# Kernel tuning notes

Hardware: AMD Instinct MI355X
Metric: run time of the kernel (lower is better)

## Reference

```python
import jax, jax.numpy as jnp
import numpy as np

N, NFEAT, NHID, NCLASS, HEADS, NLAYERS, E = 10000, 128, 64, 16, 4, 4, 160000
DT = 0.01
EPS = 1e-05


def _rmsnorm(x):
    rms = jnp.sqrt(jnp.mean(x * x, axis=-1, keepdims=True) + EPS)
    return x / rms


def setup_inputs() -> dict:
    key = jax.random.key(0)
    ks = jax.random.split(key, 16)
    s = lambda fi, fo: 1.0 / np.sqrt(fi)
    def lin(k, fi, fo):
        k1, k2 = jax.random.split(k)
        lim = 1.0 / np.sqrt(fi)
        return (jax.random.uniform(k1, (fi, fo), jnp.float32, -lim, lim),
                jax.random.uniform(k2, (fo,), jnp.float32, -lim, lim))
    x = jax.random.normal(ks[0], (N, NFEAT), jnp.float32)
    edge_index = jax.random.randint(ks[1], (2, E), 0, N, dtype=jnp.int64)
    enc_w, enc_b = lin(ks[2], NFEAT, NHID)
    dec_w, dec_b = lin(ks[3], NHID, NCLASS)
    lo_w, lo_b = lin(ks[4], NHID * HEADS, NHID)
    dpl_w, dpl_b = lin(ks[5], NHID, NHID * HEADS)
    dpr_w, dpr_b = lin(ks[6], NHID, NHID * HEADS)
    lin_w, lin_b = lin(ks[7], NHID, NHID * HEADS)
    att = jax.random.normal(ks[8], (HEADS, NHID), jnp.float32) * (1.0 / np.sqrt(NHID))
    return dict(x=x, enc_w=enc_w, enc_b=enc_b, dec_w=dec_w, dec_b=dec_b,
                lo_w=lo_w, lo_b=lo_b, dpl_w=dpl_w, dpl_b=dpl_b,
                dpr_w=dpr_w, dpr_b=dpr_b, lin_w=lin_w, lin_b=lin_b,
                att=att, edge_index=edge_index)


def reference(x, enc_w, enc_b, dec_w, dec_b, lo_w, lo_b, dpl_w, dpl_b,
              dpr_w, dpr_b, lin_w, lin_b, att, edge_index):
    row, col = edge_index[0], edge_index[1]  # src, dst

    # dynamics constants (learnable_dyn_params=False)
    omega = jax.nn.softplus(jnp.float32(1.0))
    zeta = jax.nn.softplus(jnp.float32(1.0))
    Ks = jax.nn.softplus(jnp.float32(1.0))
    omega_sq = omega * omega

    Y = jax.nn.relu(x @ enc_w + enc_b)              # [N, nhid]
    X = Y

    # fixed GATv2 attention projections from Y_0
    xl = (Y @ dpl_w + dpl_b).reshape(N, HEADS, NHID)  # [N,H,C]
    xr = (Y @ dpr_w + dpr_b).reshape(N, HEADS, NHID)

    # symmetric GCN normalization on edges
    deg = jax.ops.segment_sum(jnp.ones((E,), jnp.float32), col, num_segments=N)
    dis = jnp.where(deg > 0, deg ** -0.5, 0.0)
    norm = dis[row] * dis[col]                       # [E]

    # edge attention logits are fixed across layers (depend only on Y_0)
    e_feat = jax.nn.leaky_relu(xl[row] + xr[col], 0.2)      # [E,H,C]
    score = jnp.einsum('ehc,hc->eh', e_feat, att)           # [E,H]
    smax = jax.ops.segment_max(score, col, num_segments=N)  # [N,H]
    a = jnp.exp(score - smax[col])
    ssum = jax.ops.segment_sum(a, col, num_segments=N)      # [N,H]
    alpha = a / jnp.where(ssum[col] > 0, ssum[col], 1.0)    # [E,H]
    w_edge = alpha * norm[:, None]                          # [E,H]

    for _ in range(NLAYERS):
        v = (Y @ lin_w + lin_b).reshape(N, HEADS, NHID)     # value projection
        msg = v[row] * w_edge[:, :, None]                   # [E,H,C]
        coupling = jax.ops.segment_sum(msg, col, num_segments=N).reshape(N, HEADS * NHID)
        coupling_Y = coupling @ lo_w + lo_b                 # [N, nhid]
        Y = Y + DT * (-2.0 * zeta * omega * Y - omega_sq * X + Ks * coupling_Y)
        X = X + DT * Y
        X = _rmsnorm(X)
        Y = _rmsnorm(Y)

    return X @ dec_w + dec_b                                # [N, nclass]
```

## Files before the change

kernel.cpp:

```cpp
#include <hip/hip_runtime.h>
#include <math.h>

#define NFEAT 128
#define HC    256
#define NCLS  16
#define DT_F  0.01f
#define EPS_F 1e-5f

__device__ __forceinline__ float bf2f(unsigned short u) {
  union { unsigned int u; float f; } v; v.u = ((unsigned int)u) << 16; return v.f;
}
__device__ __forceinline__ unsigned short f2bf(float f) {
  union { float f; unsigned int u; } v; v.f = f;
  unsigned int r = v.u + 0x7fffu + ((v.u >> 16) & 1u);
  return (unsigned short)(r >> 16);
}
__device__ __forceinline__ float edge_logit(ushort4 u, float4 r4, float4 at4) {
  float vx = bf2f(u.x) + r4.x, vy = bf2f(u.y) + r4.y;
  float vz = bf2f(u.z) + r4.z, vw = bf2f(u.w) + r4.w;
  vx = fmaxf(vx, 0.2f * vx); vy = fmaxf(vy, 0.2f * vy);
  vz = fmaxf(vz, 0.2f * vz); vw = fmaxf(vw, 0.2f * vw);
  float t = vx * at4.x;
  t = fmaf(vy, at4.y, t); t = fmaf(vz, at4.z, t); t = fmaf(vw, at4.w, t);
  return t;
}

__global__ __launch_bounds__(256) void enc_kernel(
    const float* __restrict__ x, const float* __restrict__ w,
    const float* __restrict__ b, float* __restrict__ Y, float* __restrict__ X,
    unsigned short* __restrict__ Ybf, int* __restrict__ deg, int n) {
  __shared__ float ws[NFEAT * 64];
  const int gtid = blockIdx.x * 256 + threadIdx.x, GSZ = gridDim.x * 256;
  for (int t = gtid; t < n; t += GSZ) deg[t] = 0;
  for (int t = threadIdx.x; t < NFEAT * 64; t += blockDim.x) ws[t] = w[t];
  __syncthreads();
  const int wave = threadIdx.x >> 6, lane = threadIdx.x & 63;
  for (int i = blockIdx.x * 4 + wave; i < n; i += gridDim.x * 4) {
    const float* xr = x + (size_t)i * NFEAT;
    float acc = b[lane];
#pragma unroll 8
    for (int k = 0; k < NFEAT; ++k) acc = fmaf(xr[k], ws[k * 64 + lane], acc);
    acc = fmaxf(acc, 0.f);
    const size_t idx = (size_t)i * 64 + lane;
    Y[idx] = acc; X[idx] = acc; Ybf[idx] = f2bf(acc);
  }
}

__global__ __launch_bounds__(256) void proj_kernel(
    const float* __restrict__ Y,
    const float* __restrict__ wl, const float* __restrict__ bl,
    const float* __restrict__ wr, const float* __restrict__ br,
    unsigned short* __restrict__ xlb, float* __restrict__ xr, int n) {
  const int half = gridDim.x >> 1;
  const bool doR = (int)blockIdx.x < half;
  const int bid = doR ? blockIdx.x : blockIdx.x - half;
  const float* __restrict__ W = doR ? wr : wl;
  const float* __restrict__ B = doR ? br : bl;
  float wreg[64];
  const int t = threadIdx.x;
#pragma unroll
  for (int k = 0; k < 64; ++k) wreg[k] = W[k * HC + t];
  const float bias = B[t];
  for (int i0 = bid * 4; i0 < n; i0 += half * 4) {
    const float* ap = Y + (size_t)i0 * 64;
    float a0 = bias, a1 = bias, a2 = bias, a3 = bias;
#pragma unroll
    for (int k = 0; k < 64; ++k) {
      const float w = wreg[k];
      a0 = fmaf(ap[k], w, a0);
      a1 = fmaf(ap[64 + k], w, a1);
      a2 = fmaf(ap[128 + k], w, a2);
      a3 = fmaf(ap[192 + k], w, a3);
    }
    if (doR) {
      if (i0 + 0 < n) xr[(size_t)(i0 + 0) * HC + t] = a0;
      if (i0 + 1 < n) xr[(size_t)(i0 + 1) * HC + t] = a1;
      if (i0 + 2 < n) xr[(size_t)(i0 + 2) * HC + t] = a2;
      if (i0 + 3 < n) xr[(size_t)(i0 + 3) * HC + t] = a3;
    } else {
      if (i0 + 0 < n) xlb[(size_t)(i0 + 0) * HC + t] = f2bf(a0);
      if (i0 + 1 < n) xlb[(size_t)(i0 + 1) * HC + t] = f2bf(a1);
      if (i0 + 2 < n) xlb[(size_t)(i0 + 2) * HC + t] = f2bf(a2);
      if (i0 + 3 < n) xlb[(size_t)(i0 + 3) * HC + t] = f2bf(a3);
    }
  }
}

__global__ __launch_bounds__(256) void wextdeg_kernel(
    const int* __restrict__ col, const float* __restrict__ lin_w,
    const float* __restrict__ lin_b, const float* __restrict__ lo_w,
    float* __restrict__ Wext, float* __restrict__ bb, int* __restrict__ deg, int E) {
  const int gtid = blockIdx.x * 256 + threadIdx.x;
  const int GSZ = gridDim.x * 256;
  for (int e = gtid; e < E; e += GSZ) atomicAdd(&deg[col[e]], 1);
  for (int f = gtid; f < 260 * 64; f += GSZ) {
    const int b = f >> 6, j = f & 63;
    float a = 0.f;
    if (b < 256) {
      const int k = b >> 2, h = b & 3;
#pragma unroll 8
      for (int c = 0; c < 64; ++c)
        a = fmaf(lin_w[k * HC + h * 64 + c], lo_w[(size_t)(h * 64 + c) * 64 + j], a);
      Wext[b * 64 + j] = a;
    } else {
      const int h = b - 256;
#pragma unroll 8
      for (int c = 0; c < 64; ++c)
        a = fmaf(lin_b[h * 64 + c], lo_w[(size_t)(h * 64 + c) * 64 + j], a);
      bb[h * 64 + j] = a;
    }
  }
}

__global__ __launch_bounds__(1024) void scan_kernel(
    const int* __restrict__ deg, int* __restrict__ offsets, int* __restrict__ cursor,
    float* __restrict__ dis, int n) {
  __shared__ int part[1024];
  const int t = threadIdx.x;
  const int chunk = (n + 1023) / 1024;
  const int start = t * chunk;
  const int end = min(start + chunk, n);
  int s = 0;
  for (int i = start; i < end; ++i) s += deg[i];
  part[t] = s;
  __syncthreads();
  for (int off = 1; off < 1024; off <<= 1) {
    int v = (t >= off) ? part[t - off] : 0;
    __syncthreads();
    part[t] += v;
    __syncthreads();
  }
  int run = (t == 0) ? 0 : part[t - 1];
  for (int i = start; i < end; ++i) {
    offsets[i] = run;
    cursor[i] = run;
    const int d = deg[i];
    dis[i] = (d > 0) ? rsqrtf((float)d) : 0.f;
    run += d;
  }
}

__global__ __launch_bounds__(256) void scatter_kernel(
    const int* __restrict__ row, const int* __restrict__ col,
    int* __restrict__ cursor, int* __restrict__ srow, int E) {
  int e = blockIdx.x * blockDim.x + threadIdx.x;
  if (e >= E) return;
  int pos = atomicAdd(&cursor[col[e]], 1);
  srow[pos] = row[e];
}

__global__ __launch_bounds__(256) void score_layer1(
    const int* __restrict__ offs, const int* __restrict__ deg,
    const int* __restrict__ srow,
    const unsigned short* __restrict__ xlb, const float* __restrict__ xr,
    const float* __restrict__ att, const float* __restrict__ dis,
    const float* __restrict__ bb, const float* __restrict__ lo_b,
    const float* __restrict__ Wext, const unsigned short* __restrict__ ybf_in,
    const float* __restrict__ Yin, float* __restrict__ Yout,
    unsigned short* __restrict__ ybf_out, float* __restrict__ X,
    float4* __restrict__ sw, float4* __restrict__ invq, float* __restrict__ fb,
    int n, float c_decay, float c_x, float c_k) {
  const int tid = threadIdx.x, wave = tid >> 6, lane = tid & 63;
  float wreg[64];
#pragma unroll
  for (int q = 0; q < 64; ++q) wreg[q] = Wext[(wave * 64 + q) * 64 + lane];
  __shared__ float aggl[4][HC];
  __shared__ float partl[4][4][64];
  const float4 at4 = ((const float4*)att)[lane];
  const ushort4* xlb4 = (const ushort4*)xlb;
  const float4* xr4 = (const float4*)xr;
  const int i = blockIdx.x * 4 + wave;
  float g0 = 0.f, g1 = 0.f, g2 = 0.f, g3 = 0.f;
  float fbv = 0.f;
  if (i < n) {
    const int s = offs[i], e = s + deg[i];
    if (s >= e) {
      if (lane == 0) invq[i] = make_float4(0.f, 0.f, 0.f, 0.f);
      fbv = lo_b[lane];
      fb[(size_t)i * 64 + lane] = fbv;
    } else {
      const float4 r4 = xr4[(size_t)i * 64 + lane];
      const float dd = dis[i];
      float ssum = 0.f, wsum = 0.f;
      int p = s;
      int n0 = 0, n1 = 0, n2 = 0, n3 = 0;
      if (p + 3 < e) { n0 = srow[p]; n1 = srow[p + 1]; n2 = srow[p + 2]; n3 = srow[p + 3]; }
      while (p + 3 < e) {
        const int q0 = n0, q1 = n1, q2 = n2, q3 = n3;
        const int pn = p + 4;
        if (pn + 3 < e) { n0 = srow[pn]; n1 = srow[pn + 1]; n2 = srow[pn + 2]; n3 = srow[pn + 3]; }
        const ushort4 u0 = xlb4[(size_t)q0 * 64 + lane];
        const ushort4 u1 = xlb4[(size_t)q1 * 64 + lane];
        const ushort4 u2 = xlb4[(size_t)q2 * 64 + lane];
        const ushort4 u3 = xlb4[(size_t)q3 * 64 + lane];
        const float di0 = dis[q0], di1 = dis[q1], di2 = dis[q2], di3 = dis[q3];
        const float ya = bf2f(ybf_in[(size_t)q0 * 64 + lane]);
        const float yb = bf2f(ybf_in[(size_t)q1 * 64 + lane]);
        const float yc = bf2f(ybf_in[(size_t)q2 * 64 + lane]);
        const float yd = bf2f(ybf_in[(size_t)q3 * 64 + lane]);
        float t0 = edge_logit(u0, r4, at4);
        float t1 = edge_logit(u1, r4, at4);
        float t2 = edge_logit(u2, r4, at4);
        float t3 = edge_logit(u3, r4, at4);
#pragma unroll
        for (int m = 1; m < 16; m <<= 1) {
          t0 += __shfl_xor(t0, m);
          t1 += __shfl_xor(t1, m);
          t2 += __shfl_xor(t2, m);
          t3 += __shfl_xor(t3, m);
        }
        const float a0 = __expf(t0), a1 = __expf(t1), a2 = __expf(t2), a3 = __expf(t3);
        ssum += (a0 + a1) + (a2 + a3);
        const float sv0 = a0 * di0, sv1 = a1 * di1, sv2 = a2 * di2, sv3 = a3 * di3;
        wsum += (sv0 + sv1) + (sv2 + sv3);
        if ((lane & 15) == 0) {
          ((float*)&sw[p])[lane >> 4] = sv0;
          ((float*)&sw[p + 1])[lane >> 4] = sv1;
          ((float*)&sw[p + 2])[lane >> 4] = sv2;
          ((float*)&sw[p + 3])[lane >> 4] = sv3;
        }
        const float sa0 = __shfl(sv0, 0), sa1 = __shfl(sv0, 16);
        const float sa2 = __shfl(sv0, 32), sa3 = __shfl(sv0, 48);
        g0 = fmaf(sa0, ya, g0); g1 = fmaf(sa1, ya, g1);
        g2 = fmaf(sa2, ya, g2); g3 = fmaf(sa3, ya, g3);
        const float sb0 = __shfl(sv1, 0), sb1 = __shfl(sv1, 16);
        const float sb2 = __shfl(sv1, 32), sb3 = __shfl(sv1, 48);
        g0 = fmaf(sb0, yb, g0); g1 = fmaf(sb1, yb, g1);
        g2 = fmaf(sb2, yb, g2); g3 = fmaf(sb3, yb, g3);
        const float sc0 = __shfl(sv2, 0), sc1 = __shfl(sv2, 16);
        const float sc2 = __shfl(sv2, 32), sc3 = __shfl(sv2, 48);
        g0 = fmaf(sc0, yc, g0); g1 = fmaf(sc1, yc, g1);
        g2 = fmaf(sc2, yc, g2); g3 = fmaf(sc3, yc, g3);
        const float sd0 = __shfl(sv3, 0), sd1 = __shfl(sv3, 16);
        const float sd2 = __shfl(sv3, 32), sd3 = __shfl(sv3, 48);
        g0 = fmaf(sd0, yd, g0); g1 = fmaf(sd1, yd, g1);
        g2 = fmaf(sd2, yd, g2); g3 = fmaf(sd3, yd, g3);
        p = pn;
      }
      for (; p < e; ++p) {
        const int ra = srow[p];
        const ushort4 u0 = xlb4[(size_t)ra * 64 + lane];
        const float dia = dis[ra];
        const float ya = bf2f(ybf_in[(size_t)ra * 64 + lane]);
        float t0 = edge_logit(u0, r4, at4);
#pragma unroll
        for (int m = 1; m < 16; m <<= 1) t0 += __shfl_xor(t0, m);
        const float a0 = __expf(t0);
        ssum += a0;
        const float sv0 = a0 * dia;
        wsum += sv0;
        if ((lane & 15) == 0) ((float*)&sw[p])[lane >> 4] = sv0;
        const float sa0 = __shfl(sv0, 0), sa1 = __shfl(sv0, 16);
        const float sa2 = __shfl(sv0, 32), sa3 = __shfl(sv0, 48);
        g0 = fmaf(sa0, ya, g0); g1 = fmaf(sa1, ya, g1);
        g2 = fmaf(sa2, ya, g2); g3 = fmaf(sa3, ya, g3);
      }
      const float inv = dd / (ssum > 0.f ? ssum : 1.f);
      if ((lane & 15) == 0) ((float*)&invq[i])[lane >> 4] = inv;
      const float i0h = __shfl(inv, 0), i1h = __shfl(inv, 16);
      const float i2h = __shfl(inv, 32), i3h = __shfl(inv, 48);
      g0 *= i0h; g1 *= i1h; g2 *= i2h; g3 *= i3h;
      const float wqv = wsum * inv;
      const float w0 = __shfl(wqv, 0), w1 = __shfl(wqv, 16);
      const float w2 = __shfl(wqv, 32), w3 = __shfl(wqv, 48);
      fbv = lo_b[lane];
      fbv = fmaf(w0, bb[lane], fbv);
      fbv = fmaf(w1, bb[64 + lane], fbv);
      fbv = fmaf(w2, bb[128 + lane], fbv);
      fbv = fmaf(w3, bb[192 + lane], fbv);
      fb[(size_t)i * 64 + lane] = fbv;
    }
  }
  float4 o; o.x = g0; o.y = g1; o.z = g2; o.w = g3;
  ((float4*)aggl[wave])[lane] = o;
  __syncthreads();
  float p0 = 0.f, p1 = 0.f, p2 = 0.f, p3 = 0.f;
#pragma unroll
  for (int q4 = 0; q4 < 16; ++q4) {
    const float4 b0 = *(const float4*)(&aggl[0][wave * 64 + q4 * 4]);
    const float4 b1 = *(const float4*)(&aggl[1][wave * 64 + q4 * 4]);
    const float4 b2 = *(const float4*)(&aggl[2][wave * 64 + q4 * 4]);
    const float4 b3 = *(const float4*)(&aggl[3][wave * 64 + q4 * 4]);
    const float w0 = wreg[q4 * 4], w1 = wreg[q4 * 4 + 1];
    const float w2 = wreg[q4 * 4 + 2], w3 = wreg[q4 * 4 + 3];
    p0 = fmaf(b0.x, w0, p0); p0 = fmaf(b0.y, w1, p0);
    p0 = fmaf(b0.z, w2, p0); p0 = fmaf(b0.w, w3, p0);
    p1 = fmaf(b1.x, w0, p1); p1 = fmaf(b1.y, w1, p1);
    p1 = fmaf(b1.z, w2, p1); p1 = fmaf(b1.w, w3, p1);
    p2 = fmaf(b2.x, w0, p2); p2 = fmaf(b2.y, w1, p2);
    p2 = fmaf(b2.z, w2, p2); p2 = fmaf(b2.w, w3, p2);
    p3 = fmaf(b3.x, w0, p3); p3 = fmaf(b3.y, w1, p3);
    p3 = fmaf(b3.z, w2, p3); p3 = fmaf(b3.w, w3, p3);
  }
  partl[wave][0][lane] = p0;
  partl[wave][1][lane] = p1;
  partl[wave][2][lane] = p2;
  partl[wave][3][lane] = p3;
  __syncthreads();
  if (i < n) {
    const size_t idx = (size_t)i * 64 + lane;
    float outv = fbv;
    outv += partl[0][wave][lane] + partl[1][wave][lane] +
            partl[2][wave][lane] + partl[3][wave][lane];
    const float y = Yin[idx], xv = X[idx];
    const float yn = fmaf(c_k, outv, fmaf(c_x, xv, c_decay * y));
    const float xn = fmaf(DT_F, yn, xv);
    float sy = yn * yn, sx = xn * xn;
#pragma unroll
    for (int m = 32; m > 0; m >>= 1) {
      sy += __shfl_xor(sy, m);
      sx += __shfl_xor(sx, m);
    }
    const float ynn = yn * rsqrtf(sy * (1.f / 64.f) + EPS_F);
    Yout[idx] = ynn;
    ybf_out[idx] = f2bf(ynn);
    X[idx] = xn * rsqrtf(sx * (1.f / 64.f) + EPS_F);
  }
}

__global__ __launch_bounds__(256) void layer_fused(
    const int* __restrict__ offs, const int* __restrict__ deg,
    const int* __restrict__ srow,
    const float4* __restrict__ sw, const float4* __restrict__ invq,
    const unsigned short* __restrict__ ybf_in, const float* __restrict__ Wext,
    const float* __restrict__ fb, const float* __restrict__ Yin,
    float* __restrict__ Yout, unsigned short* __restrict__ ybf_out,
    float* __restrict__ X, int n, float c_decay, float c_x, float c_k) {
  const int t = threadIdx.x, tr = t >> 6, lane = t & 63;
  float wreg[64];
#pragma unroll
  for (int q = 0; q < 64; ++q) wreg[q] = Wext[(tr * 64 + q) * 64 + lane];
  __shared__ float aggl[4][HC];
  __shared__ float partl[4][4][64];
  const int i = blockIdx.x * 4 + tr;
  float4 o = make_float4(0.f, 0.f, 0.f, 0.f);
  if (i < n) {
    const int s = offs[i], e = s + deg[i];
    float a0 = 0.f, a1 = 0.f, a2 = 0.f, a3 = 0.f;
    int p = s;
    int n0 = 0, n1 = 0, n2 = 0, n3 = 0;
    if (p + 3 < e) { n0 = srow[p]; n1 = srow[p + 1]; n2 = srow[p + 2]; n3 = srow[p + 3]; }
    while (p + 3 < e) {
      const int q0 = n0, q1 = n1, q2 = n2, q3 = n3;
      const int pn = p + 4;
      if (pn + 3 < e) { n0 = srow[pn]; n1 = srow[pn + 1]; n2 = srow[pn + 2]; n3 = srow[pn + 3]; }
      const float4 v0 = sw[p], v1 = sw[p + 1], v2 = sw[p + 2], v3 = sw[p + 3];
      const float y0 = bf2f(ybf_in[(size_t)q0 * 64 + lane]);
      const float y1 = bf2f(ybf_in[(size_t)q1 * 64 + lane]);
      const float y2 = bf2f(ybf_in[(size_t)q2 * 64 + lane]);
      const float y3 = bf2f(ybf_in[(size_t)q3 * 64 + lane]);
      a0 = fmaf(v0.x, y0, a0); a1 = fmaf(v0.y, y0, a1);
      a2 = fmaf(v0.z, y0, a2); a3 = fmaf(v0.w, y0, a3);
      a0 = fmaf(v1.x, y1, a0); a1 = fmaf(v1.y, y1, a1);
      a2 = fmaf(v1.z, y1, a2); a3 = fmaf(v1.w, y1, a3);
      a0 = fmaf(v2.x, y2, a0); a1 = fmaf(v2.y, y2, a1);
      a2 = fmaf(v2.z, y2, a2); a3 = fmaf(v2.w, y2, a3);
      a0 = fmaf(v3.x, y3, a0); a1 = fmaf(v3.y, y3, a1);
      a2 = fmaf(v3.z, y3, a2); a3 = fmaf(v3.w, y3, a3);
      p = pn;
    }
    for (; p < e; ++p) {
      const int r0 = srow[p];
      const float4 v0 = sw[p];
      const float y0 = bf2f(ybf_in[(size_t)r0 * 64 + lane]);
      a0 = fmaf(v0.x, y0, a0); a1 = fmaf(v0.y, y0, a1);
      a2 = fmaf(v0.z, y0, a2); a3 = fmaf(v0.w, y0, a3);
    }
    const float4 iv = invq[i];
    o.x = a0 * iv.x; o.y = a1 * iv.y; o.z = a2 * iv.z; o.w = a3 * iv.w;
  }
  ((float4*)aggl[tr])[lane] = o;
  __syncthreads();
  float p0 = 0.f, p1 = 0.f, p2 = 0.f, p3 = 0.f;
#pragma unroll
  for (int q4 = 0; q4 < 16; ++q4) {
    const float4 b0 = *(const float4*)(&aggl[0][tr * 64 + q4 * 4]);
    const float4 b1 = *(const float4*)(&aggl[1][tr * 64 + q4 * 4]);
    const float4 b2 = *(const float4*)(&aggl[2][tr * 64 + q4 * 4]);
    const float4 b3 = *(const float4*)(&aggl[3][tr * 64 + q4 * 4]);
    const float w0 = wreg[q4 * 4], w1 = wreg[q4 * 4 + 1];
    const float w2 = wreg[q4 * 4 + 2], w3 = wreg[q4 * 4 + 3];
    p0 = fmaf(b0.x, w0, p0); p0 = fmaf(b0.y, w1, p0);
    p0 = fmaf(b0.z, w2, p0); p0 = fmaf(b0.w, w3, p0);
    p1 = fmaf(b1.x, w0, p1); p1 = fmaf(b1.y, w1, p1);
    p1 = fmaf(b1.z, w2, p1); p1 = fmaf(b1.w, w3, p1);
    p2 = fmaf(b2.x, w0, p2); p2 = fmaf(b2.y, w1, p2);
    p2 = fmaf(b2.z, w2, p2); p2 = fmaf(b2.w, w3, p2);
    p3 = fmaf(b3.x, w0, p3); p3 = fmaf(b3.y, w1, p3);
    p3 = fmaf(b3.z, w2, p3); p3 = fmaf(b3.w, w3, p3);
  }
  partl[tr][0][lane] = p0;
  partl[tr][1][lane] = p1;
  partl[tr][2][lane] = p2;
  partl[tr][3][lane] = p3;
  __syncthreads();
  if (i < n) {
    const size_t idx = (size_t)i * 64 + lane;
    float outv = fb[idx];
    outv += partl[0][tr][lane] + partl[1][tr][lane] +
            partl[2][tr][lane] + partl[3][tr][lane];
    const float y = Yin[idx], xv = X[idx];
    const float yn = fmaf(c_k, outv, fmaf(c_x, xv, c_decay * y));
    const float xn = fmaf(DT_F, yn, xv);
    float sy = yn * yn, sx = xn * xn;
#pragma unroll
    for (int m = 32; m > 0; m >>= 1) {
      sy += __shfl_xor(sy, m);
      sx += __shfl_xor(sx, m);
    }
    const float ynn = yn * rsqrtf(sy * (1.f / 64.f) + EPS_F);
    Yout[idx] = ynn;
    ybf_out[idx] = f2bf(ynn);
    X[idx] = xn * rsqrtf(sx * (1.f / 64.f) + EPS_F);
  }
}

__global__ __launch_bounds__(256) void layer_last_dec(
    const int* __restrict__ offs, const int* __restrict__ deg,
    const int* __restrict__ srow,
    const float4* __restrict__ sw, const float4* __restrict__ invq,
    const unsigned short* __restrict__ ybf_in, const float* __restrict__ Wext,
    const float* __restrict__ fb, const float* __restrict__ Yin,
    const float* __restrict__ X,
    const float* __restrict__ dec_w, const float* __restrict__ dec_b,
    float* __restrict__ out, int n, float c_decay, float c_x, float c_k) {
  const int t = threadIdx.x, tr = t >> 6, lane = t & 63;
  float wreg[64];
#pragma unroll
  for (int q = 0; q < 64; ++q) wreg[q] = Wext[(tr * 64 + q) * 64 + lane];
  __shared__ float aggl[4][HC];
  __shared__ float partl[4][4][64];
  const int i = blockIdx.x * 4 + tr;
  float4 o = make_float4(0.f, 0.f, 0.f, 0.f);
  if (i < n) {
    const int s = offs[i], e = s + deg[i];
    float a0 = 0.f, a1 = 0.f, a2 = 0.f, a3 = 0.f;
    int p = s;
    int n0 = 0, n1 = 0, n2 = 0, n3 = 0;
    if (p + 3 < e) { n0 = srow[p]; n1 = srow[p + 1]; n2 = srow[p + 2]; n3 = srow[p + 3]; }
    while (p + 3 < e) {
      const int q0 = n0, q1 = n1, q2 = n2, q3 = n3;
      const int pn = p + 4;
      if (pn + 3 < e) { n0 = srow[pn]; n1 = srow[pn + 1]; n2 = srow[pn + 2]; n3 = srow[pn + 3]; }
      const float4 v0 = sw[p], v1 = sw[p + 1], v2 = sw[p + 2], v3 = sw[p + 3];
      const float y0 = bf2f(ybf_in[(size_t)q0 * 64 + lane]);
      const float y1 = bf2f(ybf_in[(size_t)q1 * 64 + lane]);
      const float y2 = bf2f(ybf_in[(size_t)q2 * 64 + lane]);
      const float y3 = bf2f(ybf_in[(size_t)q3 * 64 + lane]);
      a0 = fmaf(v0.x, y0, a0); a1 = fmaf(v0.y, y0, a1);
      a2 = fmaf(v0.z, y0, a2); a3 = fmaf(v0.w, y0, a3);
      a0 = fmaf(v1.x, y1, a0); a1 = fmaf(v1.y, y1, a1);
      a2 = fmaf(v1.z, y1, a2); a3 = fmaf(v1.w, y1, a3);
      a0 = fmaf(v2.x, y2, a0); a1 = fmaf(v2.y, y2, a1);
      a2 = fmaf(v2.z, y2, a2); a3 = fmaf(v2.w, y2, a3);
      a0 = fmaf(v3.x, y3, a0); a1 = fmaf(v3.y, y3, a1);
      a2 = fmaf(v3.z, y3, a2); a3 = fmaf(v3.w, y3, a3);
      p = pn;
    }
    for (; p < e; ++p) {
      const int r0 = srow[p];
      const float4 v0 = sw[p];
      const float y0 = bf2f(ybf_in[(size_t)r0 * 64 + lane]);
      a0 = fmaf(v0.x, y0, a0); a1 = fmaf(v0.y, y0, a1);
      a2 = fmaf(v0.z, y0, a2); a3 = fmaf(v0.w, y0, a3);
    }
    const float4 iv = invq[i];
    o.x = a0 * iv.x; o.y = a1 * iv.y; o.z = a2 * iv.z; o.w = a3 * iv.w;
  }
  ((float4*)aggl[tr])[lane] = o;
  __syncthreads();
  float p0 = 0.f, p1 = 0.f, p2 = 0.f, p3 = 0.f;
#pragma unroll
  for (int q4 = 0; q4 < 16; ++q4) {
    const float4 b0 = *(const float4*)(&aggl[0][tr * 64 + q4 * 4]);
    const float4 b1 = *(const float4*)(&aggl[1][tr * 64 + q4 * 4]);
    const float4 b2 = *(const float4*)(&aggl[2][tr * 64 + q4 * 4]);
    const float4 b3 = *(const float4*)(&aggl[3][tr * 64 + q4 * 4]);
    const float w0 = wreg[q4 * 4], w1 = wreg[q4 * 4 + 1];
    const float w2 = wreg[q4 * 4 + 2], w3 = wreg[q4 * 4 + 3];
    p0 = fmaf(b0.x, w0, p0); p0 = fmaf(b0.y, w1, p0);
    p0 = fmaf(b0.z, w2, p0); p0 = fmaf(b0.w, w3, p0);
    p1 = fmaf(b1.x, w0, p1); p1 = fmaf(b1.y, w1, p1);
    p1 = fmaf(b1.z, w2, p1); p1 = fmaf(b1.w, w3, p1);
    p2 = fmaf(b2.x, w0, p2); p2 = fmaf(b2.y, w1, p2);
    p2 = fmaf(b2.z, w2, p2); p2 = fmaf(b2.w, w3, p2);
    p3 = fmaf(b3.x, w0, p3); p3 = fmaf(b3.y, w1, p3);
    p3 = fmaf(b3.z, w2, p3); p3 = fmaf(b3.w, w3, p3);
  }
  partl[tr][0][lane] = p0;
  partl[tr][1][lane] = p1;
  partl[tr][2][lane] = p2;
  partl[tr][3][lane] = p3;
  __syncthreads();
  if (i < n) {
    const size_t idx = (size_t)i * 64 + lane;
    float outv = fb[idx];
    outv += partl[0][tr][lane] + partl[1][tr][lane] +
            partl[2][tr][lane] + partl[3][tr][lane];
    const float y = Yin[idx], xv = X[idx];
    const float yn = fmaf(c_k, outv, fmaf(c_x, xv, c_decay * y));
    const float xn = fmaf(DT_F, yn, xv);
    float sx = xn * xn;
#pragma unroll
    for (int m = 32; m > 0; m >>= 1) sx += __shfl_xor(sx, m);
    const float xnn = xn * rsqrtf(sx * (1.f / 64.f) + EPS_F);
    aggl[tr][lane] = xnn;
    const int j = lane & 15, kq = lane >> 4;
    float a = 0.f;
#pragma unroll
    for (int k2 = 0; k2 < 16; ++k2) {
      const int k = kq * 16 + k2;
      a = fmaf(aggl[tr][k], dec_w[k * NCLS + j], a);
    }
    a += __shfl_xor(a, 16);
    a += __shfl_xor(a, 32);
    if (lane < 16) out[(size_t)i * NCLS + lane] = a + dec_b[lane];
  }
}

static inline size_t alignup(size_t x) { return (x + 255) & ~(size_t)255; }

extern "C" void kernel_launch(void* const* d_in, const int* in_sizes, int n_in,
                              void* d_out, int out_size, void* d_ws, size_t ws_size,
                              hipStream_t stream) {
  const float* x     = (const float*)d_in[0];
  const float* enc_w = (const float*)d_in[1];
  const float* enc_b = (const float*)d_in[2];
  const float* dec_w = (const float*)d_in[3];
  const float* dec_b = (const float*)d_in[4];
  const float* lo_w  = (const float*)d_in[5];
  const float* lo_b  = (const float*)d_in[6];
  const float* dpl_w = (const float*)d_in[7];
  const float* dpl_b = (const float*)d_in[8];
  const float* dpr_w = (const float*)d_in[9];
  const float* dpr_b = (const float*)d_in[10];
  const float* lin_w = (const float*)d_in[11];
  const float* lin_b = (const float*)d_in[12];
  const float* att   = (const float*)d_in[13];
  const int*   ei    = (const int*)d_in[14];

  const int n = in_sizes[0] / NFEAT;
  const int E = in_sizes[14] / 2;
  const int* row = ei;
  const int* col = ei + E;

  char* p = (char*)d_ws;
  size_t off = 0;
  auto alloc = [&](size_t bytes) { void* r = p + off; off += alignup(bytes); return r; };
  float*          Y    = (float*)alloc((size_t)n * 64 * 4);
  float*          Y2   = (float*)alloc((size_t)n * 64 * 4);
  float*          X    = (float*)alloc((size_t)n * 64 * 4);
  unsigned short* ybfA = (unsigned short*)alloc((size_t)n * 64 * 2);
  unsigned short* ybfB = (unsigned short*)alloc((size_t)n * 64 * 2);
  unsigned short* xlb  = (unsigned short*)alloc((size_t)n * HC * 2);
  float*          xr   = (float*)alloc((size_t)n * HC * 4);
  float4*         sw   = (float4*)alloc((size_t)E * 16);
  int*            srow = (int*)alloc((size_t)E * 4);
  int*            deg  = (int*)alloc((size_t)n * 4);
  int*            offs = (int*)alloc((size_t)(n + 1) * 4);
  int*            cur  = (int*)alloc((size_t)n * 4);
  float*          dis  = (float*)alloc((size_t)n * 4);
  float4*         invq = (float4*)alloc((size_t)n * 16);
  float*          fb   = (float*)alloc((size_t)n * 64 * 4);
  float*          Wext = (float*)alloc((size_t)HC * 64 * 4);
  float*          bb   = (float*)alloc((size_t)HC * 4);

  const double sp = log1p(exp(1.0));
  const float c_decay = (float)(1.0 - 2.0 * sp * sp * 0.01);
  const float c_x     = (float)(-(sp * sp) * 0.01);
  const float c_k     = (float)(sp * 0.01);

  const int quads = (n + 3) / 4;

  enc_kernel<<<512, 256, 0, stream>>>(x, enc_w, enc_b, Y, X, ybfA, deg, n);
  proj_kernel<<<1024, 256, 0, stream>>>(Y, dpl_w, dpl_b, dpr_w, dpr_b, xlb, xr, n);
  wextdeg_kernel<<<512, 256, 0, stream>>>(col, lin_w, lin_b, lo_w, Wext, bb, deg, E);
  scan_kernel<<<1, 1024, 0, stream>>>(deg, offs, cur, dis, n);
  scatter_kernel<<<(E + 255) / 256, 256, 0, stream>>>(row, col, cur, srow, E);
  score_layer1<<<quads, 256, 0, stream>>>(offs, deg, srow, xlb, xr, att, dis, bb, lo_b,
                                          Wext, ybfA, Y, Y2, ybfB, X, sw, invq, fb,
                                          n, c_decay, c_x, c_k);
  layer_fused<<<quads, 256, 0, stream>>>(offs, deg, srow, sw, invq, ybfB, Wext, fb,
                                         Y2, Y, ybfA, X, n, c_decay, c_x, c_k);
  layer_fused<<<quads, 256, 0, stream>>>(offs, deg, srow, sw, invq, ybfA, Wext, fb,
                                         Y, Y2, ybfB, X, n, c_decay, c_x, c_k);
  layer_last_dec<<<quads, 256, 0, stream>>>(offs, deg, srow, sw, invq, ybfB, Wext, fb,
                                            Y2, X, dec_w, dec_b, (float*)d_out,
                                            n, c_decay, c_x, c_k);
}
```

Baseline: 202.4 us.

## Store gathered Y and xl features in fp8 and merge weight-prep into projection kernel

Changes the gathered per-node buffers (Y copies and the xl attention projection) from bf16 to fp8 e4m3 using the hardware convert builtins, halving gather bytes in the edge-aggregation kernels. Also folds the degree counting and the Wext/bb weight precompute into the projection kernel, removing one launch. Fp8 cuts precision on the attention logits and messages, which may push outputs past the tolerance.

```diff
diff --git a/kernel.cpp b/kernel.cpp
--- a/kernel.cpp
+++ b/kernel.cpp
@@ -7,17 +7,21 @@
 #define DT_F  0.01f
 #define EPS_F 1e-5f
 
-__device__ __forceinline__ float bf2f(unsigned short u) {
-  union { unsigned int u; float f; } v; v.u = ((unsigned int)u) << 16; return v.f;
-}
-__device__ __forceinline__ unsigned short f2bf(float f) {
-  union { float f; unsigned int u; } v; v.f = f;
-  unsigned int r = v.u + 0x7fffu + ((v.u >> 16) & 1u);
-  return (unsigned short)(r >> 16);
-}
-__device__ __forceinline__ float edge_logit(ushort4 u, float4 r4, float4 at4) {
-  float vx = bf2f(u.x) + r4.x, vy = bf2f(u.y) + r4.y;
-  float vz = bf2f(u.z) + r4.z, vw = bf2f(u.w) + r4.w;
+__device__ __forceinline__ unsigned char f2f8(float f) {
+  int v = __builtin_amdgcn_cvt_pk_fp8_f32(f, f, 0, false);
+  return (unsigned char)(v & 0xff);
+}
+__device__ __forceinline__ float f82f(unsigned int b) {
+  return __builtin_amdgcn_cvt_f32_fp8((int)b, 0);
+}
+__device__ __forceinline__ float f82f_sel0(unsigned int w) { return __builtin_amdgcn_cvt_f32_fp8((int)w, 0); }
+__device__ __forceinline__ float f82f_sel1(unsigned int w) { return __builtin_amdgcn_cvt_f32_fp8((int)w, 1); }
+__device__ __forceinline__ float f82f_sel2(unsigned int w) { return __builtin_amdgcn_cvt_f32_fp8((int)w, 2); }
+__device__ __forceinline__ float f82f_sel3(unsigned int w) { return __builtin_amdgcn_cvt_f32_fp8((int)w, 3); }
+
+__device__ __forceinline__ float edge_logit(unsigned int w, float4 r4, float4 at4) {
+  float vx = f82f_sel0(w) + r4.x, vy = f82f_sel1(w) + r4.y;
+  float vz = f82f_sel2(w) + r4.z, vw = f82f_sel3(w) + r4.w;
   vx = fmaxf(vx, 0.2f * vx); vy = fmaxf(vy, 0.2f * vy);
   vz = fmaxf(vz, 0.2f * vz); vw = fmaxf(vw, 0.2f * vw);
   float t = vx * at4.x;
@@ -28,7 +32,7 @@
 __global__ __launch_bounds__(256) void enc_kernel(
     const float* __restrict__ x, const float* __restrict__ w,
     const float* __restrict__ b, float* __restrict__ Y, float* __restrict__ X,
-    unsigned short* __restrict__ Ybf, int* __restrict__ deg, int n) {
+    unsigned char* __restrict__ Ybf, int* __restrict__ deg, int n) {
   __shared__ float ws[NFEAT * 64];
   const int gtid = blockIdx.x * 256 + threadIdx.x, GSZ = gridDim.x * 256;
   for (int t = gtid; t < n; t += GSZ) deg[t] = 0;
@@ -42,7 +46,7 @@
     for (int k = 0; k < NFEAT; ++k) acc = fmaf(xr[k], ws[k * 64 + lane], acc);
     acc = fmaxf(acc, 0.f);
     const size_t idx = (size_t)i * 64 + lane;
-    Y[idx] = acc; X[idx] = acc; Ybf[idx] = f2bf(acc);
+    Y[idx] = acc; X[idx] = acc; Ybf[idx] = f2f8(acc);
   }
 }
 
@@ -50,7 +54,11 @@
     const float* __restrict__ Y,
     const float* __restrict__ wl, const float* __restrict__ bl,
     const float* __restrict__ wr, const float* __restrict__ br,
-    unsigned short* __restrict__ xlb, float* __restrict__ xr, int n) {
+    const int* __restrict__ col, const float* __restrict__ lin_w,
+    const float* __restrict__ lin_b, const float* __restrict__ lo_w,
+    unsigned char* __restrict__ xlb, float* __restrict__ xr,
+    float* __restrict__ Wext, float* __restrict__ bb, int* __restrict__ deg,
+    int n, int E) {
   const int half = gridDim.x >> 1;
   const bool doR = (int)blockIdx.x < half;
   const int bid = doR ? blockIdx.x : blockIdx.x - half;
@@ -78,32 +86,25 @@
       if (i0 + 2 < n) xr[(size_t)(i0 + 2) * HC + t] = a2;
       if (i0 + 3 < n) xr[(size_t)(i0 + 3) * HC + t] = a3;
     } else {
-      if (i0 + 0 < n) xlb[(size_t)(i0 + 0) * HC + t] = f2bf(a0);
-      if (i0 + 1 < n) xlb[(size_t)(i0 + 1) * HC + t] = f2bf(a1);
-      if (i0 + 2 < n) xlb[(size_t)(i0 + 2) * HC + t] = f2bf(a2);
-      if (i0 + 3 < n) xlb[(size_t)(i0 + 3) * HC + t] = f2bf(a3);
-    }
-  }
-}
-
-__global__ __launch_bounds__(256) void wextdeg_kernel(
-    const int* __restrict__ col, const float* __restrict__ lin_w,
-    const float* __restrict__ lin_b, const float* __restrict__ lo_w,
-    float* __restrict__ Wext, float* __restrict__ bb, int* __restrict__ deg, int E) {
-  const int gtid = blockIdx.x * 256 + threadIdx.x;
-  const int GSZ = gridDim.x * 256;
+      if (i0 + 0 < n) xlb[(size_t)(i0 + 0) * HC + t] = f2f8(a0);
+      if (i0 + 1 < n) xlb[(size_t)(i0 + 1) * HC + t] = f2f8(a1);
+      if (i0 + 2 < n) xlb[(size_t)(i0 + 2) * HC + t] = f2f8(a2);
+      if (i0 + 3 < n) xlb[(size_t)(i0 + 3) * HC + t] = f2f8(a3);
+    }
+  }
+  const int gtid = blockIdx.x * 256 + t, GSZ = gridDim.x * 256;
   for (int e = gtid; e < E; e += GSZ) atomicAdd(&deg[col[e]], 1);
   for (int f = gtid; f < 260 * 64; f += GSZ) {
-    const int b = f >> 6, j = f & 63;
+    const int b2 = f >> 6, j = f & 63;
     float a = 0.f;
-    if (b < 256) {
-      const int k = b >> 2, h = b & 3;
+    if (b2 < 256) {
+      const int k = b2 >> 2, h = b2 & 3;
 #pragma unroll 8
       for (int c = 0; c < 64; ++c)
         a = fmaf(lin_w[k * HC + h * 64 + c], lo_w[(size_t)(h * 64 + c) * 64 + j], a);
-      Wext[b * 64 + j] = a;
+      Wext[b2 * 64 + j] = a;
     } else {
-      const int h = b - 256;
+      const int h = b2 - 256;
 #pragma unroll 8
       for (int c = 0; c < 64; ++c)
         a = fmaf(lin_b[h * 64 + c], lo_w[(size_t)(h * 64 + c) * 64 + j], a);
@@ -152,12 +153,12 @@
 __global__ __launch_bounds__(256) void score_layer1(
     const int* __restrict__ offs, const int* __restrict__ deg,
     const int* __restrict__ srow,
-    const unsigned short* __restrict__ xlb, const float* __restrict__ xr,
+    const unsigned char* __restrict__ xlb, const float* __restrict__ xr,
     const float* __restrict__ att, const float* __restrict__ dis,
     const float* __restrict__ bb, const float* __restrict__ lo_b,
-    const float* __restrict__ Wext, const unsigned short* __restrict__ ybf_in,
+    const float* __restrict__ Wext, const unsigned char* __restrict__ ybf_in,
     const float* __restrict__ Yin, float* __restrict__ Yout,
-    unsigned short* __restrict__ ybf_out, float* __restrict__ X,
+    unsigned char* __restrict__ ybf_out, float* __restrict__ X,
     float4* __restrict__ sw, float4* __restrict__ invq, float* __restrict__ fb,
     int n, float c_decay, float c_x, float c_k) {
   const int tid = threadIdx.x, wave = tid >> 6, lane = tid & 63;
@@ -167,7 +168,7 @@
   __shared__ float aggl[4][HC];
   __shared__ float partl[4][4][64];
   const float4 at4 = ((const float4*)att)[lane];
-  const ushort4* xlb4 = (const ushort4*)xlb;
+  const unsigned int* xlb4 = (const unsigned int*)xlb;
   const float4* xr4 = (const float4*)xr;
   const int i = blockIdx.x * 4 + wave;
   float g0 = 0.f, g1 = 0.f, g2 = 0.f, g3 = 0.f;
@@ -189,15 +190,15 @@
         const int q0 = n0, q1 = n1, q2 = n2, q3 = n3;
         const int pn = p + 4;
         if (pn + 3 < e) { n0 = srow[pn]; n1 = srow[pn + 1]; n2 = srow[pn + 2]; n3 = srow[pn + 3]; }
-        const ushort4 u0 = xlb4[(size_t)q0 * 64 + lane];
-        const ushort4 u1 = xlb4[(size_t)q1 * 64 + lane];
-        const ushort4 u2 = xlb4[(size_t)q2 * 64 + lane];
-        const ushort4 u3 = xlb4[(size_t)q3 * 64 + lane];
+        const unsigned int u0 = xlb4[(size_t)q0 * 64 + lane];
+        const unsigned int u1 = xlb4[(size_t)q1 * 64 + lane];
+        const unsigned int u2 = xlb4[(size_t)q2 * 64 + lane];
+        const unsigned int u3 = xlb4[(size_t)q3 * 64 + lane];
         const float di0 = dis[q0], di1 = dis[q1], di2 = dis[q2], di3 = dis[q3];
-        const float ya = bf2f(ybf_in[(size_t)q0 * 64 + lane]);
-        const float yb = bf2f(ybf_in[(size_t)q1 * 64 + lane]);
-        const float yc = bf2f(ybf_in[(size_t)q2 * 64 + lane]);
-        const float yd = bf2f(ybf_in[(size_t)q3 * 64 + lane]);
+        const float ya = f82f(ybf_in[(size_t)q0 * 64 + lane]);
+        const float yb = f82f(ybf_in[(size_t)q1 * 64 + lane]);
+        const float yc = f82f(ybf_in[(size_t)q2 * 64 + lane]);
+        const float yd = f82f(ybf_in[(size_t)q3 * 64 + lane]);
         float t0 = edge_logit(u0, r4, at4);
         float t1 = edge_logit(u1, r4, at4);
         float t2 = edge_logit(u2, r4, at4);
@@ -239,9 +240,9 @@
       }
       for (; p < e; ++p) {
         const int ra = srow[p];
-        const ushort4 u0 = xlb4[(size_t)ra * 64 + lane];
+        const unsigned int u0 = xlb4[(size_t)ra * 64 + lane];
         const float dia = dis[ra];
-        const float ya = bf2f(ybf_in[(size_t)ra * 64 + lane]);
+        const float ya = f82f(ybf_in[(size_t)ra * 64 + lane]);
         float t0 = edge_logit(u0, r4, at4);
 #pragma unroll
         for (int m = 1; m < 16; m <<= 1) t0 += __shfl_xor(t0, m);
@@ -313,7 +314,7 @@
     }
     const float ynn = yn * rsqrtf(sy * (1.f / 64.f) + EPS_F);
     Yout[idx] = ynn;
-    ybf_out[idx] = f2bf(ynn);
+    ybf_out[idx] = f2f8(ynn);
     X[idx] = xn * rsqrtf(sx * (1.f / 64.f) + EPS_F);
   }
 }
@@ -322,9 +323,9 @@
     const int* __restrict__ offs, const int* __restrict__ deg,
     const int* __restrict__ srow,
     const float4* __restrict__ sw, const float4* __restrict__ invq,
-    const unsigned short* __restrict__ ybf_in, const float* __restrict__ Wext,
+    const unsigned char* __restrict__ ybf_in, const float* __restrict__ Wext,
     const float* __restrict__ fb, const float* __restrict__ Yin,
-    float* __restrict__ Yout, unsigned short* __restrict__ ybf_out,
+    float* __restrict__ Yout, unsigned char* __restrict__ ybf_out,
     float* __restrict__ X, int n, float c_decay, float c_x, float c_k) {
   const int t = threadIdx.x, tr = t >> 6, lane = t & 63;
   float wreg[64];
@@ -345,10 +346,10 @@
       const int pn = p + 4;
       if (pn + 3 < e) { n0 = srow[pn]; n1 = srow[pn + 1]; n2 = srow[pn + 2]; n3 = srow[pn + 3]; }
       const float4 v0 = sw[p], v1 = sw[p + 1], v2 = sw[p + 2], v3 = sw[p + 3];
-      const float y0 = bf2f(ybf_in[(size_t)q0 * 64 + lane]);
-      const float y1 = bf2f(ybf_in[(size_t)q1 * 64 + lane]);
-      const float y2 = bf2f(ybf_in[(size_t)q2 * 64 + lane]);
-      const float y3 = bf2f(ybf_in[(size_t)q3 * 64 + lane]);
+      const float y0 = f82f(ybf_in[(size_t)q0 * 64 + lane]);
+      const float y1 = f82f(ybf_in[(size_t)q1 * 64 + lane]);
+      const float y2 = f82f(ybf_in[(size_t)q2 * 64 + lane]);
+      const float y3 = f82f(ybf_in[(size_t)q3 * 64 + lane]);
       a0 = fmaf(v0.x, y0, a0); a1 = fmaf(v0.y, y0, a1);
       a2 = fmaf(v0.z, y0, a2); a3 = fmaf(v0.w, y0, a3);
       a0 = fmaf(v1.x, y1, a0); a1 = fmaf(v1.y, y1, a1);
@@ -362,7 +363,7 @@
     for (; p < e; ++p) {
       const int r0 = srow[p];
       const float4 v0 = sw[p];
-      const float y0 = bf2f(ybf_in[(size_t)r0 * 64 + lane]);
+      const float y0 = f82f(ybf_in[(size_t)r0 * 64 + lane]);
       a0 = fmaf(v0.x, y0, a0); a1 = fmaf(v0.y, y0, a1);
       a2 = fmaf(v0.z, y0, a2); a3 = fmaf(v0.w, y0, a3);
     }
@@ -410,7 +411,7 @@
     }
     const float ynn = yn * rsqrtf(sy * (1.f / 64.f) + EPS_F);
     Yout[idx] = ynn;
-    ybf_out[idx] = f2bf(ynn);
+    ybf_out[idx] = f2f8(ynn);
     X[idx] = xn * rsqrtf(sx * (1.f / 64.f) + EPS_F);
   }
 }
@@ -419,7 +420,7 @@
     const int* __restrict__ offs, const int* __restrict__ deg,
     const int* __restrict__ srow,
     const float4* __restrict__ sw, const float4* __restrict__ invq,
-    const unsigned short* __restrict__ ybf_in, const float* __restrict__ Wext,
+    const unsigned char* __restrict__ ybf_in, const float* __restrict__ Wext,
     const float* __restrict__ fb, const float* __restrict__ Yin,
     const float* __restrict__ X,
     const float* __restrict__ dec_w, const float* __restrict__ dec_b,
@@ -443,10 +444,10 @@
       const int pn = p + 4;
       if (pn + 3 < e) { n0 = srow[pn]; n1 = srow[pn + 1]; n2 = srow[pn + 2]; n3 = srow[pn + 3]; }
       const float4 v0 = sw[p], v1 = sw[p + 1], v2 = sw[p + 2], v3 = sw[p + 3];
-      const float y0 = bf2f(ybf_in[(size_t)q0 * 64 + lane]);
-      const float y1 = bf2f(ybf_in[(size_t)q1 * 64 + lane]);
-      const float y2 = bf2f(ybf_in[(size_t)q2 * 64 + lane]);
-      const float y3 = bf2f(ybf_in[(size_t)q3 * 64 + lane]);
+      const float y0 = f82f(ybf_in[(size_t)q0 * 64 + lane]);
+      const float y1 = f82f(ybf_in[(size_t)q1 * 64 + lane]);
+      const float y2 = f82f(ybf_in[(size_t)q2 * 64 + lane]);
+      const float y3 = f82f(ybf_in[(size_t)q3 * 64 + lane]);
       a0 = fmaf(v0.x, y0, a0); a1 = fmaf(v0.y, y0, a1);
       a2 = fmaf(v0.z, y0, a2); a3 = fmaf(v0.w, y0, a3);
       a0 = fmaf(v1.x, y1, a0); a1 = fmaf(v1.y, y1, a1);
@@ -460,7 +461,7 @@
     for (; p < e; ++p) {
       const int r0 = srow[p];
       const float4 v0 = sw[p];
-      const float y0 = bf2f(ybf_in[(size_t)r0 * 64 + lane]);
+      const float y0 = f82f(ybf_in[(size_t)r0 * 64 + lane]);
       a0 = fmaf(v0.x, y0, a0); a1 = fmaf(v0.y, y0, a1);
       a2 = fmaf(v0.z, y0, a2); a3 = fmaf(v0.w, y0, a3);
     }
@@ -547,23 +548,23 @@
   char* p = (char*)d_ws;
   size_t off = 0;
   auto alloc = [&](size_t bytes) { void* r = p + off; off += alignup(bytes); return r; };
-  float*          Y    = (float*)alloc((size_t)n * 64 * 4);
-  float*          Y2   = (float*)alloc((size_t)n * 64 * 4);
-  float*          X    = (float*)alloc((size_t)n * 64 * 4);
-  unsigned short* ybfA = (unsigned short*)alloc((size_t)n * 64 * 2);
-  unsigned short* ybfB = (unsigned short*)alloc((size_t)n * 64 * 2);
-  unsigned short* xlb  = (unsigned short*)alloc((size_t)n * HC * 2);
-  float*          xr   = (float*)alloc((size_t)n * HC * 4);
-  float4*         sw   = (float4*)alloc((size_t)E * 16);
-  int*            srow = (int*)alloc((size_t)E * 4);
-  int*            deg  = (int*)alloc((size_t)n * 4);
-  int*            offs = (int*)alloc((size_t)(n + 1) * 4);
-  int*            cur  = (int*)alloc((size_t)n * 4);
-  float*          dis  = (float*)alloc((size_t)n * 4);
-  float4*         invq = (float4*)alloc((size_t)n * 16);
-  float*          fb   = (float*)alloc((size_t)n * 64 * 4);
-  float*          Wext = (float*)alloc((size_t)HC * 64 * 4);
-  float*          bb   = (float*)alloc((size_t)HC * 4);
+  float*         Y    = (float*)alloc((size_t)n * 64 * 4);
+  float*         Y2   = (float*)alloc((size_t)n * 64 * 4);
+  float*         X    = (float*)alloc((size_t)n * 64 * 4);
+  unsigned char* ybfA = (unsigned char*)alloc((size_t)n * 64);
+  unsigned char* ybfB = (unsigned char*)alloc((size_t)n * 64);
+  unsigned char* xlb  = (unsigned char*)alloc((size_t)n * HC);
+  float*         xr   = (float*)alloc((size_t)n * HC * 4);
+  float4*        sw   = (float4*)alloc((size_t)E * 16);
+  int*           srow = (int*)alloc((size_t)E * 4);
+  int*           deg  = (int*)alloc((size_t)n * 4);
+  int*           offs = (int*)alloc((size_t)(n + 1) * 4);
+  int*           cur  = (int*)alloc((size_t)n * 4);
+  float*         dis  = (float*)alloc((size_t)n * 4);
+  float4*        invq = (float4*)alloc((size_t)n * 16);
+  float*         fb   = (float*)alloc((size_t)n * 64 * 4);
+  float*         Wext = (float*)alloc((size_t)HC * 64 * 4);
+  float*         bb   = (float*)alloc((size_t)HC * 4);
 
   const double sp = log1p(exp(1.0));
   const float c_decay = (float)(1.0 - 2.0 * sp * sp * 0.01);
@@ -573,8 +574,9 @@
   const int quads = (n + 3) / 4;
 
   enc_kernel<<<512, 256, 0, stream>>>(x, enc_w, enc_b, Y, X, ybfA, deg, n);
-  proj_kernel<<<1024, 256, 0, stream>>>(Y, dpl_w, dpl_b, dpr_w, dpr_b, xlb, xr, n);
-  wextdeg_kernel<<<512, 256, 0, stream>>>(col, lin_w, lin_b, lo_w, Wext, bb, deg, E);
+  proj_kernel<<<1024, 256, 0, stream>>>(Y, dpl_w, dpl_b, dpr_w, dpr_b, col,
+                                        lin_w, lin_b, lo_w, xlb, xr, Wext, bb, deg,
+                                        n, E);
   scan_kernel<<<1, 1024, 0, stream>>>(deg, offs, cur, dis, n);
   scatter_kernel<<<(E + 255) / 256, 256, 0, stream>>>(row, col, cur, srow, E);
   score_layer1<<<quads, 256, 0, stream>>>(offs, deg, srow, xlb, xr, att, dis, bb, lo_b,
```

New measurement: 190.1 us. 6.1% less time.
